# Optimization experiments

Measured on AMD Instinct MI355X. Metric: run time of the kernel, lower is better.

Reference implementation:

```python
import jax, jax.numpy as jnp
import numpy as np

B, T_TEXT, T_MEL = 8, 256, 1024
VOCAB, MEL, H = 256, 80, 512
NH, HD = 8, 64  # MultiheadAttention: 8 heads, head_dim 64


def _linear(x, w, b):
    return x @ w.T + b


def _lstm(x, w_ih, w_hh, b_ih, b_hh, reverse=False):
    # torch LSTM, gate order i,f,g,o; x: [B,T,Din] -> [B,T,H]
    xg = jnp.einsum('bti,gi->btg', x, w_ih) + b_ih  # precompute input contributions
    h0 = jnp.zeros((x.shape[0], w_hh.shape[1]), x.dtype)

    def step(carry, xt):
        h, c = carry
        g = xt + h @ w_hh.T + b_hh
        i, f, gg, o = jnp.split(g, 4, axis=-1)
        c = jax.nn.sigmoid(f) * c + jax.nn.sigmoid(i) * jnp.tanh(gg)
        h = jax.nn.sigmoid(o) * jnp.tanh(c)
        return (h, c), h

    _, hs = jax.lax.scan(step, (h0, h0), jnp.swapaxes(xg, 0, 1), reverse=reverse)
    return jnp.swapaxes(hs, 0, 1)


def _length_regulate(enc, durations, max_len):
    # Vectorized equivalent of the nested python loop: token j owns output
    # positions [cum[j-1], cum[j]); padded positions are zero, mask True=pad.
    dur = jnp.round(durations).astype(jnp.int32)
    cum = jnp.cumsum(dur, axis=1)                              # [B,T_text]
    pos = jnp.arange(max_len)                                  # [max_len]
    idx = jax.vmap(lambda c: jnp.searchsorted(c, pos, side='right'))(cum)
    pad_mask = pos[None, :] >= cum[:, -1:]                     # True = padded
    idx = jnp.minimum(idx, enc.shape[1] - 1)
    exp = jnp.take_along_axis(enc, idx[..., None], axis=1)     # [B,max_len,H]
    exp = exp * (~pad_mask)[..., None].astype(enc.dtype)
    return exp, pad_mask


def setup_inputs() -> dict:
    key = jax.random.key(0)
    ks = jax.random.split(key, 40)

    def rn(k, shape, scale=0.02):
        return jax.random.normal(k, shape, jnp.float32) * scale

    inp = {}
    inp['phoneme_indices'] = jax.random.randint(ks[0], (B, T_TEXT), 0, VOCAB)
    inp['mel_specs'] = jax.random.normal(ks[1], (B, T_MEL, MEL), jnp.float32)
    inp['phoneme_durations'] = jax.random.randint(ks[2], (B, T_TEXT), 0, 8).astype(jnp.float32)
    # parameters
    inp['emb'] = rn(ks[3], (VOCAB, H), 1.0)
    inp['enc_w_ih_f'] = rn(ks[4], (4 * H, H))
    inp['enc_w_hh_f'] = rn(ks[5], (4 * H, H))
    inp['enc_b_ih_f'] = rn(ks[6], (4 * H,))
    inp['enc_b_hh_f'] = rn(ks[7], (4 * H,))
    inp['enc_w_ih_b'] = rn(ks[8], (4 * H, H))
    inp['enc_w_hh_b'] = rn(ks[9], (4 * H, H))
    inp['enc_b_ih_b'] = rn(ks[10], (4 * H,))
    inp['enc_b_hh_b'] = rn(ks[11], (4 * H,))
    inp['proj_w'] = rn(ks[12], (H, 2 * H))
    inp['proj_b'] = rn(ks[13], (H,))
    inp['dur_w1'] = rn(ks[14], (H, H))
    inp['dur_b1'] = rn(ks[15], (H,))
    inp['dur_w2'] = rn(ks[16], (H // 2, H))
    inp['dur_b2'] = rn(ks[17], (H // 2,))
    inp['dur_w3'] = rn(ks[18], (1, H // 2))
    inp['dur_b3'] = rn(ks[19], (1,))
    inp['mel_in_w'] = rn(ks[20], (H, MEL))
    inp['mel_in_b'] = rn(ks[21], (H,))
    inp['attn_in_w'] = rn(ks[22], (3 * H, H))
    inp['attn_in_b'] = rn(ks[23], (3 * H,))
    inp['attn_out_w'] = rn(ks[24], (H, H))
    inp['attn_out_b'] = rn(ks[25], (H,))
    inp['dec_w_ih'] = rn(ks[26], (4 * H, 2 * H))
    inp['dec_w_hh'] = rn(ks[27], (4 * H, H))
    inp['dec_b_ih'] = rn(ks[28], (4 * H,))
    inp['dec_b_hh'] = rn(ks[29], (4 * H,))
    inp['mel_out_w'] = rn(ks[30], (MEL, H))
    inp['mel_out_b'] = rn(ks[31], (MEL,))
    return inp


def reference(phoneme_indices, mel_specs, phoneme_durations, emb,
              enc_w_ih_f, enc_w_hh_f, enc_b_ih_f, enc_b_hh_f,
              enc_w_ih_b, enc_w_hh_b, enc_b_ih_b, enc_b_hh_b,
              proj_w, proj_b, dur_w1, dur_b1, dur_w2, dur_b2, dur_w3, dur_b3,
              mel_in_w, mel_in_b, attn_in_w, attn_in_b, attn_out_w, attn_out_b,
              dec_w_ih, dec_w_hh, dec_b_ih, dec_b_hh, mel_out_w, mel_out_b):
    b = phoneme_indices.shape[0]
    # encode_text (dropout = identity in eval)
    x = emb[phoneme_indices]                                   # [B,T_text,H]
    hf = _lstm(x, enc_w_ih_f, enc_w_hh_f, enc_b_ih_f, enc_b_hh_f)
    hb = _lstm(x, enc_w_ih_b, enc_w_hh_b, enc_b_ih_b, enc_b_hh_b, reverse=True)
    enc = _linear(jnp.concatenate([hf, hb], axis=-1), proj_w, proj_b)
    # duration predictor
    h1 = jax.nn.relu(_linear(enc, dur_w1, dur_b1))
    h2 = jax.nn.relu(_linear(h1, dur_w2, dur_b2))
    log_dur = _linear(h2, dur_w3, dur_b3)[..., 0]              # [B,T_text]
    # length regulation to mel length
    exp, pad_mask = _length_regulate(enc, phoneme_durations, mel_specs.shape[1])
    # teacher-forced decoder: queries depend only on shifted mel targets,
    # so the per-timestep attention loop == one batched MHA over all steps.
    mel_in = jnp.concatenate([jnp.zeros_like(mel_specs[:, :1]), mel_specs[:, :-1]], axis=1)
    q_in = _linear(mel_in, mel_in_w, mel_in_b)                 # [B,T_mel,H]
    wq, wk, wv = jnp.split(attn_in_w, 3, axis=0)
    bq, bk, bv = jnp.split(attn_in_b, 3, axis=0)
    q = _linear(q_in, wq, bq).reshape(b, -1, NH, HD)
    k = _linear(exp, wk, bk).reshape(b, -1, NH, HD)
    v = _linear(exp, wv, bv).reshape(b, -1, NH, HD)
    scores = jnp.einsum('bqhd,bkhd->bhqk', q, k) / np.sqrt(HD).astype(np.float32)
    scores = jnp.where(pad_mask[:, None, None, :], jnp.asarray(-1e9, scores.dtype), scores)
    attn = jax.nn.softmax(scores, axis=-1)
    ctx = jnp.einsum('bhqk,bkhd->bqhd', attn, v).reshape(b, -1, H)
    attended = _linear(ctx, attn_out_w, attn_out_b)
    # decoder LSTM over full sequence (the only true recurrence)
    dec_in = jnp.concatenate([q_in, attended], axis=-1)        # [B,T_mel,2H]
    dec_out = _lstm(dec_in, dec_w_ih, dec_w_hh, dec_b_ih, dec_b_hh)
    mel_pred = _linear(dec_out, mel_out_w, mel_out_b)          # [B,T_mel,MEL]
    return mel_pred, log_dur
```

## Files before the change

kernel.cpp:

```cpp
#include <hip/hip_runtime.h>
#include <hip/hip_bf16.h>


typedef unsigned short u16;
typedef unsigned int u32;
typedef unsigned long long u64;
typedef short short8 __attribute__((ext_vector_type(8)));
typedef float float4_ __attribute__((ext_vector_type(4)));

__device__ __forceinline__ u16 f2b16(float f) {
  u32 u = __float_as_uint(f);
  u = (u + 0x7FFF + ((u >> 16) & 1)) >> 16;
  return (u16)u;
}
__device__ __forceinline__ float b2f(u16 h) { return __uint_as_float((u32)h << 16); }
__device__ __forceinline__ float sigm(float x) { return 1.f / (1.f + __expf(-x)); }
__device__ __forceinline__ float tanh_(float x) { return 2.f / (1.f + __expf(-2.f * x)) - 1.f; }

__global__ void f2b_k(const float* __restrict__ s, u16* __restrict__ d, int n) {
  for (int i = blockIdx.x * 256 + threadIdx.x; i < n; i += gridDim.x * 256) d[i] = f2b16(s[i]);
}
__global__ void permconv_k(const float* __restrict__ s, u16* __restrict__ d, int K) {
  int row = blockIdx.x; int u = row >> 2, G = row & 3;
  const float* sr = s + (long)(G * 512 + u) * K;
  u16* dr = d + (long)row * K;
  for (int c = threadIdx.x; c < K; c += 256) dr[c] = f2b16(sr[c]);
}
__global__ void biascomb_k(const float* __restrict__ bih, const float* __restrict__ bhh,
                           float* __restrict__ out) {
  int r = blockIdx.x * 256 + threadIdx.x;
  int u = r >> 2, G = r & 3;
  out[r] = bih[G * 512 + u] + bhh[G * 512 + u];
}
__global__ void melinw_k(const float* __restrict__ s, u16* __restrict__ d) {
  int row = blockIdx.x, c = threadIdx.x;
  d[row * 128 + c] = (c < 80) ? f2b16(s[row * 80 + c]) : (u16)0;
}
__global__ void meloutw_k(const float* __restrict__ s, u16* __restrict__ d) {
  int row = blockIdx.x;
  for (int c = threadIdx.x; c < 512; c += 256)
    d[row * 512 + c] = (row < 80) ? f2b16(s[row * 512 + c]) : (u16)0;
}
__global__ void biaspad_k(const float* __restrict__ s, float* __restrict__ d) {
  int t = threadIdx.x;
  d[t] = (t < 80) ? s[t] : 0.f;
}
__global__ void embed_k(const int* __restrict__ pid, const float* __restrict__ emb,
                        u16* __restrict__ x) {
  int t = blockIdx.x, b = blockIdx.y;
  int row = pid[b * 256 + t];
  const float* e = emb + (long)row * 512;
  u16* xr = x + ((long)b * 256 + t) * 512;
  xr[threadIdx.x] = f2b16(e[threadIdx.x]);
  xr[threadIdx.x + 256] = f2b16(e[threadIdx.x + 256]);
}
__global__ void melin_k(const float* __restrict__ mel, u16* __restrict__ out) {
  int t = blockIdx.x, b = blockIdx.y, c = threadIdx.x;
  float v = (c < 80 && t > 0) ? mel[((long)b * 1024 + (t - 1)) * 80 + c] : 0.f;
  out[((long)b * 1024 + t) * 128 + c] = f2b16(v);
}
__global__ void cumsum_k(const float* __restrict__ dur, int* __restrict__ cum,
                         int* __restrict__ Lb) {
  int b = blockIdx.x, t = threadIdx.x;
  __shared__ int sd[256];
  sd[t] = __float2int_rn(dur[b * 256 + t]);
  __syncthreads();
  for (int o = 1; o < 256; o <<= 1) {
    int v = (t >= o) ? sd[t - o] : 0;
    __syncthreads();
    sd[t] += v;
    __syncthreads();
  }
  cum[b * 256 + t] = sd[t];
  if (t == 255) Lb[b] = min(sd[255], 1024);
}
__global__ void gather_k(const int* __restrict__ cum, const u16* __restrict__ enc,
                         u16* __restrict__ exp_) {
  int pos = blockIdx.x, b = blockIdx.y;
  const int* cb = cum + b * 256;
  int last = cb[255];
  u32 val = 0;
  if (pos < last) {
    int lo = 0, hi = 255;
    while (lo < hi) { int mid = (lo + hi) >> 1; if (cb[mid] > pos) hi = mid; else lo = mid + 1; }
    val = ((const u32*)(enc + ((long)b * 256 + lo) * 512))[threadIdx.x];
  }
  ((u32*)(exp_ + ((long)b * 1024 + pos) * 512))[threadIdx.x] = val;
}
__global__ void softmax_k(const float* __restrict__ sbuf, u16* __restrict__ P,
                          const int* __restrict__ Lb) {
  int qp = blockIdx.x, b = blockIdx.y;
  const float* s = sbuf + ((long)b * 1024 + qp) * 1024;
  u16* p = P + ((long)b * 1024 + qp) * 1024;
  int L = Lb[b];
  __shared__ float red[256];
  int tid = threadIdx.x;
  float m = -1e30f;
  for (int i = tid; i < L; i += 256) m = fmaxf(m, s[i]);
  red[tid] = m; __syncthreads();
  for (int o = 128; o > 0; o >>= 1) { if (tid < o) red[tid] = fmaxf(red[tid], red[tid + o]); __syncthreads(); }
  float mx = red[0];
  __syncthreads();
  float sm = 0.f;
  for (int i = tid; i < L; i += 256) sm += __expf(s[i] - mx);
  red[tid] = sm; __syncthreads();
  for (int o = 128; o > 0; o >>= 1) { if (tid < o) red[tid] += red[tid + o]; __syncthreads(); }
  float inv = 1.f / red[0];
  for (int i = tid; i < 1024; i += 256) {
    float v = (i < L) ? __expf(s[i] - mx) * inv : 0.f;
    p[i] = f2b16(v);
  }
}
__global__ void dur3_k(const u16* __restrict__ h2, const float* __restrict__ w3,
                       const float* __restrict__ b3, float* __restrict__ out) {
  int row = blockIdx.x * 4 + (threadIdx.x >> 6);
  int l = threadIdx.x & 63;
  const u16* hr = h2 + (long)row * 256;
  float s = 0.f;
  for (int i = 0; i < 4; i++) { int c = l * 4 + i; s += b2f(hr[c]) * w3[c]; }
  for (int o = 32; o > 0; o >>= 1) s += __shfl_down(s, o);
  if (l == 0) out[row] = s + b3[0];
}

__global__ __launch_bounds__(256) void gemm_bt(
    const u16* __restrict__ A, const u16* __restrict__ A2, int ksplit, int lda, int lda2, long sA,
    const u16* __restrict__ B, int ldb, long sB, void* __restrict__ Cv, int ldc, long sC,
    const float* __restrict__ bias, float alpha, int N, int K, int flags) {
  __shared__ u16 As[128 * 72];
  __shared__ u16 Bs[128 * 72];
  int z = blockIdx.z;
  const u16* Ab = A + (long)z * sA;
  const u16* A2b = A2 ? (A2 + (long)z * sA) : (const u16*)0;
  const u16* Bb = B + (long)z * sB;
  int m0 = blockIdx.x * 128, n0 = blockIdx.y * 128;
  int tid = threadIdx.x, wave = tid >> 6, lane = tid & 63;
  int wm = wave & 1, wn = wave >> 1;
  int nl = lane & 15, kb = (lane >> 4) * 8, ml = (lane >> 4) * 4;
  float4_ acc[4][4];
  for (int i = 0; i < 4; i++)
    for (int j = 0; j < 4; j++) { acc[i][j][0] = 0; acc[i][j][1] = 0; acc[i][j][2] = 0; acc[i][j][3] = 0; }
  int rr = tid >> 3, cc = (tid & 7) * 8;
  for (int k0 = 0; k0 < K; k0 += 64) {
    int gk = k0 + cc;
#pragma unroll
    for (int i = 0; i < 4; i++) {
      int row = rr + i * 32;
      const u16* sa = (gk < ksplit) ? (Ab + (long)(m0 + row) * lda + gk)
                                    : (A2b + (long)(m0 + row) * lda2 + (gk - ksplit));
      *(short8*)&As[row * 72 + cc] = *(const short8*)sa;
      *(short8*)&Bs[row * 72 + cc] = *(const short8*)(Bb + (long)(n0 + row) * ldb + gk);
    }
    __syncthreads();
#pragma unroll
    for (int kk = 0; kk < 64; kk += 32) {
      short8 af[4], bfr[4];
#pragma unroll
      for (int i = 0; i < 4; i++) af[i] = *(const short8*)&As[(wm * 64 + i * 16 + nl) * 72 + kk + kb];
#pragma unroll
      for (int i = 0; i < 4; i++) bfr[i] = *(const short8*)&Bs[(wn * 64 + i * 16 + nl) * 72 + kk + kb];
#pragma unroll
      for (int mi = 0; mi < 4; mi++)
#pragma unroll
        for (int ni = 0; ni < 4; ni++)
          acc[mi][ni] = __builtin_amdgcn_mfma_f32_16x16x32_bf16(af[mi], bfr[ni], acc[mi][ni], 0, 0, 0);
    }
    __syncthreads();
  }
  for (int ni = 0; ni < 4; ni++) {
    int n = n0 + wn * 64 + ni * 16 + nl;
    if (n >= N) continue;
    float bv = bias ? bias[n] : 0.f;
    for (int mi = 0; mi < 4; mi++) {
#pragma unroll
      for (int r = 0; r < 4; r++) {
        int m = m0 + wm * 64 + mi * 16 + ml + r;
        float v = acc[mi][ni][r] * alpha + bv;
        if (flags & 2) v = fmaxf(v, 0.f);
        long idx = (flags & 4) ? ((long)n * ldc + m) : ((long)m * ldc + n);
        if (flags & 1) ((u16*)Cv)[z * sC + idx] = f2b16(v);
        else ((float*)Cv)[z * sC + idx] = v;
      }
    }
  }
}


__global__ __launch_bounds__(256) void enc_rec_k(
    const float* __restrict__ xg_f, const float* __restrict__ xg_b,
    const u16* __restrict__ whh_f, const u16* __restrict__ whh_b,
    u16* __restrict__ hcat, u64* __restrict__ hglob) {
  int dir = blockIdx.x >> 5, wg = blockIdx.x & 31;
  int tid = threadIdx.x, wave = tid >> 6, lane = tid & 63;
  int nl = lane & 15, kb = (lane >> 4) * 8, ml = (lane >> 4) * 4;
  int nt = wg * 4 + wave;
  const float* xg = dir ? xg_b : xg_f;
  const u16* whh = dir ? whh_b : whh_f;
  u64* hg = hglob + dir * 4096;
  __shared__ u16 h_s[2][16 * 520];
  __shared__ float gbuf[4][16][17];
  __shared__ float c_s[4][4][8];
  short8 warr[16];
  {
    const u16* wr = whh + (long)(wg * 64 + wave * 16 + nl) * 512 + kb;
#pragma unroll
    for (int kc = 0; kc < 16; kc++) warr[kc] = *(const short8*)(wr + kc * 32);
  }
  if (lane < 32) c_s[wave][lane & 3][lane >> 2] = 0.f;
  __syncthreads();
  float nxt[4];
  {
    int t0 = dir ? 255 : 0;
#pragma unroll
    for (int r = 0; r < 4; r++) {
      int m = ml + r;
      nxt[r] = (m < 8) ? xg[((long)m * 256 + t0) * 2048 + nt * 16 + nl] : 0.f;
    }
  }
  int prow = tid >> 5, c32 = tid & 31;
  for (int s = 0; s < 256; ++s) {
    int t = dir ? 255 - s : s;
    int pb = s & 1;
    float cur0 = nxt[0], cur1 = nxt[1], cur2 = nxt[2], cur3 = nxt[3];
    if (s > 0) {
      const u64* hp = hg + (long)pb * 2048 + prow * 256 + c32 * 2;
      u64 a[8];
      u32 tg = (u32)s;
      for (;;) {
#pragma unroll
        for (int j = 0; j < 4; j++) {
          a[2 * j] = __hip_atomic_load(hp + j * 64, __ATOMIC_RELAXED, __HIP_MEMORY_SCOPE_AGENT);
          a[2 * j + 1] =
              __hip_atomic_load(hp + j * 64 + 1, __ATOMIC_RELAXED, __HIP_MEMORY_SCOPE_AGENT);
        }
        u32 bad = 0;
#pragma unroll
        for (int i = 0; i < 8; i++) bad |= ((u32)(a[i] >> 32) ^ tg);
        if (!bad) break;
      }
      u64* dp = (u64*)(h_s[pb] + prow * 520);
#pragma unroll
      for (int j = 0; j < 4; j++)
        dp[c32 + j * 32] = (a[2 * j] & 0xffffffffull) | (a[2 * j + 1] << 32);
    }
    __syncthreads();
    if (s + 1 < 256) {
      int tn = dir ? 255 - (s + 1) : (s + 1);
#pragma unroll
      for (int r = 0; r < 4; r++) {
        int m = ml + r;
        nxt[r] = (m < 8) ? xg[((long)m * 256 + tn) * 2048 + nt * 16 + nl] : 0.f;
      }
    }
    float4_ ac0, ac1, ac2, ac3;
    ac0[0] = cur0; ac0[1] = cur1; ac0[2] = cur2; ac0[3] = cur3;
    ac1[0] = 0; ac1[1] = 0; ac1[2] = 0; ac1[3] = 0;
    ac2 = ac1; ac3 = ac1;
    if (s > 0) {
      const u16* hrow = h_s[pb] + nl * 520 + kb;
#pragma unroll
      for (int kc = 0; kc < 16; kc += 4) {
        ac0 = __builtin_amdgcn_mfma_f32_16x16x32_bf16(
            *(const short8*)(hrow + (kc + 0) * 32), warr[kc + 0], ac0, 0, 0, 0);
        ac1 = __builtin_amdgcn_mfma_f32_16x16x32_bf16(
            *(const short8*)(hrow + (kc + 1) * 32), warr[kc + 1], ac1, 0, 0, 0);
        ac2 = __builtin_amdgcn_mfma_f32_16x16x32_bf16(
            *(const short8*)(hrow + (kc + 2) * 32), warr[kc + 2], ac2, 0, 0, 0);
        ac3 = __builtin_amdgcn_mfma_f32_16x16x32_bf16(
            *(const short8*)(hrow + (kc + 3) * 32), warr[kc + 3], ac3, 0, 0, 0);
      }
    }
    float4_ acc = (ac0 + ac1) + (ac2 + ac3);
    gbuf[wave][nl][ml + 0] = acc[0];
    gbuf[wave][nl][ml + 1] = acc[1];
    gbuf[wave][nl][ml + 2] = acc[2];
    gbuf[wave][nl][ml + 3] = acc[3];
    if (lane < 32) {
      int ul = lane & 3, b = lane >> 2;
      float gi = gbuf[wave][ul * 4 + 0][b];
      float gf = gbuf[wave][ul * 4 + 1][b];
      float gg = gbuf[wave][ul * 4 + 2][b];
      float go = gbuf[wave][ul * 4 + 3][b];
      float c = c_s[wave][ul][b];
      c = sigm(gf) * c + sigm(gi) * tanh_(gg);
      float h = sigm(go) * tanh_(c);
      c_s[wave][ul][b] = c;
      int u = nt * 4 + ul;
      u16 hb2 = f2b16(h);
      u32 partner = (u32)__shfl_down((int)hb2, 1);
      if ((ul & 1) == 0) {
        u32 pair = (u32)hb2 | (partner << 16);
        *(u32*)&hcat[((long)b * 256 + t) * 1024 + dir * 512 + u] = pair;
        u64 word = (u64)pair | ((u64)(u32)(s + 1) << 32);
        __hip_atomic_store(hg + (long)((s + 1) & 1) * 2048 + b * 256 + (u >> 1), word,
                           __ATOMIC_RELAXED, __HIP_MEMORY_SCOPE_AGENT);
      }
    }
  }
}

__global__ __launch_bounds__(256) void dec_rec_k(
    const float* __restrict__ xg, const u16* __restrict__ whh,
    u16* __restrict__ dec_out, u64* __restrict__ hglob) {
  int wg = blockIdx.x;
  int tid = threadIdx.x, wave = tid >> 6, lane = tid & 63;
  int nl = lane & 15, kb = (lane >> 4) * 8, ml = (lane >> 4) * 4;
  int nt = wg * 4 + wave;
  __shared__ u16 h_s[2][16 * 520];
  __shared__ float gbuf[4][16][17];
  __shared__ float c_s[4][4][8];
  short8 warr[16];
  {
    const u16* wr = whh + (long)(wg * 64 + wave * 16 + nl) * 512 + kb;
#pragma unroll
    for (int kc = 0; kc < 16; kc++) warr[kc] = *(const short8*)(wr + kc * 32);
  }
  if (lane < 32) c_s[wave][lane & 3][lane >> 2] = 0.f;
  __syncthreads();
  float nxt[4];
#pragma unroll
  for (int r = 0; r < 4; r++) {
    int m = ml + r;
    nxt[r] = (m < 8) ? xg[((long)m * 1024 + 0) * 2048 + nt * 16 + nl] : 0.f;
  }
  int prow = tid >> 5, c32 = tid & 31;
  for (int s = 0; s < 1024; ++s) {
    int pb = s & 1;
    float cur0 = nxt[0], cur1 = nxt[1], cur2 = nxt[2], cur3 = nxt[3];
    if (s > 0) {
      const u64* hp = hglob + (long)pb * 2048 + prow * 256 + c32 * 2;
      u64 a[8];
      u32 tg = (u32)s;
      for (;;) {
#pragma unroll
        for (int j = 0; j < 4; j++) {
          a[2 * j] = __hip_atomic_load(hp + j * 64, __ATOMIC_RELAXED, __HIP_MEMORY_SCOPE_AGENT);
          a[2 * j + 1] =
              __hip_atomic_load(hp + j * 64 + 1, __ATOMIC_RELAXED, __HIP_MEMORY_SCOPE_AGENT);
        }
        u32 bad = 0;
#pragma unroll
        for (int i = 0; i < 8; i++) bad |= ((u32)(a[i] >> 32) ^ tg);
        if (!bad) break;
      }
      u64* dp = (u64*)(h_s[pb] + prow * 520);
#pragma unroll
      for (int j = 0; j < 4; j++)
        dp[c32 + j * 32] = (a[2 * j] & 0xffffffffull) | (a[2 * j + 1] << 32);
    }
    __syncthreads();
    if (s + 1 < 1024) {
#pragma unroll
      for (int r = 0; r < 4; r++) {
        int m = ml + r;
        nxt[r] = (m < 8) ? xg[((long)m * 1024 + (s + 1)) * 2048 + nt * 16 + nl] : 0.f;
      }
    }
    float4_ ac0, ac1, ac2, ac3;
    ac0[0] = cur0; ac0[1] = cur1; ac0[2] = cur2; ac0[3] = cur3;
    ac1[0] = 0; ac1[1] = 0; ac1[2] = 0; ac1[3] = 0;
    ac2 = ac1; ac3 = ac1;
    if (s > 0) {
      const u16* hrow = h_s[pb] + nl * 520 + kb;
#pragma unroll
      for (int kc = 0; kc < 16; kc += 4) {
        ac0 = __builtin_amdgcn_mfma_f32_16x16x32_bf16(
            *(const short8*)(hrow + (kc + 0) * 32), warr[kc + 0], ac0, 0, 0, 0);
        ac1 = __builtin_amdgcn_mfma_f32_16x16x32_bf16(
            *(const short8*)(hrow + (kc + 1) * 32), warr[kc + 1], ac1, 0, 0, 0);
        ac2 = __builtin_amdgcn_mfma_f32_16x16x32_bf16(
            *(const short8*)(hrow + (kc + 2) * 32), warr[kc + 2], ac2, 0, 0, 0);
        ac3 = __builtin_amdgcn_mfma_f32_16x16x32_bf16(
            *(const short8*)(hrow + (kc + 3) * 32), warr[kc + 3], ac3, 0, 0, 0);
      }
    }
    float4_ acc = (ac0 + ac1) + (ac2 + ac3);
    gbuf[wave][nl][ml + 0] = acc[0];
    gbuf[wave][nl][ml + 1] = acc[1];
    gbuf[wave][nl][ml + 2] = acc[2];
    gbuf[wave][nl][ml + 3] = acc[3];
    if (lane < 32) {
      int ul = lane & 3, b = lane >> 2;
      float gi = gbuf[wave][ul * 4 + 0][b];
      float gf = gbuf[wave][ul * 4 + 1][b];
      float gg = gbuf[wave][ul * 4 + 2][b];
      float go = gbuf[wave][ul * 4 + 3][b];
      float c = c_s[wave][ul][b];
      c = sigm(gf) * c + sigm(gi) * tanh_(gg);
      float h = sigm(go) * tanh_(c);
      c_s[wave][ul][b] = c;
      int u = nt * 4 + ul;
      u16 hb2 = f2b16(h);
      u32 partner = (u32)__shfl_down((int)hb2, 1);
      if ((ul & 1) == 0) {
        u32 pair = (u32)hb2 | (partner << 16);
        *(u32*)&dec_out[((long)b * 1024 + s) * 512 + u] = pair;
        u64 word = (u64)pair | ((u64)(u32)(s + 1) << 32);
        __hip_atomic_store(hglob + (long)((s + 1) & 1) * 2048 + b * 256 + (u >> 1), word,
                           __ATOMIC_RELAXED, __HIP_MEMORY_SCOPE_AGENT);
      }
    }
  }
}

extern "C" void kernel_launch(void* const* d_in, const int* in_sizes, int n_in,
                              void* d_out, int out_size, void* d_ws, size_t ws_size,
                              hipStream_t stream) {
  (void)in_sizes; (void)n_in; (void)out_size; (void)ws_size;
  const int* pid = (const int*)d_in[0];
  const float* mel = (const float*)d_in[1];
  const float* dur = (const float*)d_in[2];
  const float* emb = (const float*)d_in[3];
  const float* e_ihf = (const float*)d_in[4];
  const float* e_hhf = (const float*)d_in[5];
  const float* e_bihf = (const float*)d_in[6];
  const float* e_bhhf = (const float*)d_in[7];
  const float* e_ihb = (const float*)d_in[8];
  const float* e_hhb = (const float*)d_in[9];
  const float* e_bihb = (const float*)d_in[10];
  const float* e_bhhb = (const float*)d_in[11];
  const float* proj_w = (const float*)d_in[12];
  const float* proj_b = (const float*)d_in[13];
  const float* dw1 = (const float*)d_in[14];
  const float* db1 = (const float*)d_in[15];
  const float* dw2 = (const float*)d_in[16];
  const float* db2 = (const float*)d_in[17];
  const float* dw3 = (const float*)d_in[18];
  const float* db3 = (const float*)d_in[19];
  const float* miw = (const float*)d_in[20];
  const float* mib = (const float*)d_in[21];
  const float* aiw = (const float*)d_in[22];
  const float* aib = (const float*)d_in[23];
  const float* aow = (const float*)d_in[24];
  const float* aob = (const float*)d_in[25];
  const float* d_ih = (const float*)d_in[26];
  const float* d_hh = (const float*)d_in[27];
  const float* d_bih = (const float*)d_in[28];
  const float* d_bhh = (const float*)d_in[29];
  const float* mow = (const float*)d_in[30];
  const float* mob = (const float*)d_in[31];
  float* out = (float*)d_out;

  char* W = (char*)d_ws;
  constexpr size_t o_xgf = 0;
  constexpr size_t o_xgb = o_xgf + 16777216;
  constexpr size_t o_sbuf = o_xgb + 16777216;
  constexpr size_t o_decxg = o_xgf;
  constexpr size_t o_pool = o_sbuf + 33554432;
  constexpr size_t o_x = o_pool;
  constexpr size_t o_hcat = o_x + 2097152;
  constexpr size_t o_dh1 = o_hcat + 4194304;
  constexpr size_t o_dh2 = o_dh1 + 2097152;
  constexpr size_t o_melin = o_dh2 + 1048576;
  constexpr size_t o_att = o_pool;
  constexpr size_t o_enc = o_melin + 2097152;
  constexpr size_t o_exp = o_enc + 2097152;
  constexpr size_t o_ctx = o_exp;
  constexpr size_t o_qin = o_exp + 8388608;
  constexpr size_t o_q = o_qin + 8388608;
  constexpr size_t o_decout = o_q;
  constexpr size_t o_k = o_q + 8388608;
  constexpr size_t o_vt = o_k + 8388608;
  constexpr size_t o_p = o_vt + 8519680;
  constexpr size_t o_w0 = o_p + 16777216;
  constexpr size_t o_w_eihf = o_w0;
  constexpr size_t o_w_eihb = o_w_eihf + 2097152;
  constexpr size_t o_w_ehhf = o_w_eihb + 2097152;
  constexpr size_t o_w_ehhb = o_w_ehhf + 2097152;
  constexpr size_t o_w_dih = o_w_ehhb + 2097152;
  constexpr size_t o_w_dhh = o_w_dih + 4194304;
  constexpr size_t o_w_proj = o_w_dhh + 2097152;
  constexpr size_t o_w_d1 = o_w_proj + 1048576;
  constexpr size_t o_w_d2 = o_w_d1 + 524288;
  constexpr size_t o_w_ai = o_w_d2 + 262144;
  constexpr size_t o_w_ao = o_w_ai + 1572864;
  constexpr size_t o_w_mi = o_w_ao + 524288;
  constexpr size_t o_w_mo = o_w_mi + 131072;
  constexpr size_t o_bc_ef = o_w_mo + 131072;
  constexpr size_t o_bc_eb = o_bc_ef + 8192;
  constexpr size_t o_bc_d = o_bc_eb + 8192;
  constexpr size_t o_b_mo = o_bc_d + 8192;
  constexpr size_t o_cum = o_b_mo + 512;
  constexpr size_t o_lb = o_cum + 8192;
  constexpr size_t o_hge = o_lb + 256;
  constexpr size_t o_hgd = o_hge + 65536;

  hipMemsetAsync(W + o_hge, 0, 98304, stream);

  f2b_k<<<512, 256, 0, stream>>>(proj_w, (u16*)(W + o_w_proj), 512 * 1024);
  f2b_k<<<512, 256, 0, stream>>>(dw1, (u16*)(W + o_w_d1), 512 * 512);
  f2b_k<<<256, 256, 0, stream>>>(dw2, (u16*)(W + o_w_d2), 256 * 512);
  f2b_k<<<512, 256, 0, stream>>>(aiw, (u16*)(W + o_w_ai), 1536 * 512);
  f2b_k<<<512, 256, 0, stream>>>(aow, (u16*)(W + o_w_ao), 512 * 512);
  permconv_k<<<2048, 256, 0, stream>>>(e_ihf, (u16*)(W + o_w_eihf), 512);
  permconv_k<<<2048, 256, 0, stream>>>(e_ihb, (u16*)(W + o_w_eihb), 512);
  permconv_k<<<2048, 256, 0, stream>>>(e_hhf, (u16*)(W + o_w_ehhf), 512);
  permconv_k<<<2048, 256, 0, stream>>>(e_hhb, (u16*)(W + o_w_ehhb), 512);
  permconv_k<<<2048, 256, 0, stream>>>(d_ih, (u16*)(W + o_w_dih), 1024);
  permconv_k<<<2048, 256, 0, stream>>>(d_hh, (u16*)(W + o_w_dhh), 512);
  biascomb_k<<<8, 256, 0, stream>>>(e_bihf, e_bhhf, (float*)(W + o_bc_ef));
  biascomb_k<<<8, 256, 0, stream>>>(e_bihb, e_bhhb, (float*)(W + o_bc_eb));
  biascomb_k<<<8, 256, 0, stream>>>(d_bih, d_bhh, (float*)(W + o_bc_d));
  melinw_k<<<512, 128, 0, stream>>>(miw, (u16*)(W + o_w_mi));
  meloutw_k<<<128, 256, 0, stream>>>(mow, (u16*)(W + o_w_mo));
  biaspad_k<<<1, 128, 0, stream>>>(mob, (float*)(W + o_b_mo));

  auto gemm = [&](size_t oA, size_t oA2, int ksplit, int lda, int lda2, long sA, size_t oB,
                  int ldb, long sB, void* C, int ldc, long sC, const float* bias, float alpha,
                  int M, int N, int K, int flags, int batch) {
    dim3 g(M / 128, (N + 127) / 128, batch);
    gemm_bt<<<g, 256, 0, stream>>>((const u16*)(W + oA),
                                   oA2 ? (const u16*)(W + oA2) : (const u16*)0, ksplit, lda, lda2,
                                   sA, (const u16*)(W + oB), ldb, sB, C, ldc, sC, bias, alpha, N,
                                   K, flags);
  };

  embed_k<<<dim3(256, 8), 256, 0, stream>>>(pid, emb, (u16*)(W + o_x));
  gemm(o_x, 0, 512, 512, 0, 0, o_w_eihf, 512, 0, W + o_xgf, 2048, 0,
       (const float*)(W + o_bc_ef), 1.f, 2048, 2048, 512, 0, 1);
  gemm(o_x, 0, 512, 512, 0, 0, o_w_eihb, 512, 0, W + o_xgb, 2048, 0,
       (const float*)(W + o_bc_eb), 1.f, 2048, 2048, 512, 0, 1);
  enc_rec_k<<<64, 256, 0, stream>>>((const float*)(W + o_xgf), (const float*)(W + o_xgb),
                                    (const u16*)(W + o_w_ehhf), (const u16*)(W + o_w_ehhb),
                                    (u16*)(W + o_hcat), (u64*)(W + o_hge));
  gemm(o_hcat, 0, 1024, 1024, 0, 0, o_w_proj, 1024, 0, W + o_enc, 512, 0, proj_b, 1.f, 2048, 512,
       1024, 1, 1);
  gemm(o_enc, 0, 512, 512, 0, 0, o_w_d1, 512, 0, W + o_dh1, 512, 0, db1, 1.f, 2048, 512, 512, 3, 1);
  gemm(o_dh1, 0, 512, 512, 0, 0, o_w_d2, 512, 0, W + o_dh2, 256, 0, db2, 1.f, 2048, 256, 512, 3, 1);
  dur3_k<<<512, 256, 0, stream>>>((const u16*)(W + o_dh2), dw3, db3, out + 655360);
  cumsum_k<<<8, 256, 0, stream>>>(dur, (int*)(W + o_cum), (int*)(W + o_lb));
  gather_k<<<dim3(1024, 8), 256, 0, stream>>>((const int*)(W + o_cum), (const u16*)(W + o_enc),
                                              (u16*)(W + o_exp));
  melin_k<<<dim3(1024, 8), 128, 0, stream>>>(mel, (u16*)(W + o_melin));
  gemm(o_melin, 0, 128, 128, 0, 0, o_w_mi, 128, 0, W + o_qin, 512, 0, mib, 1.f, 8192, 512, 128, 1, 1);
  gemm(o_qin, 0, 512, 512, 0, 0, o_w_ai, 512, 0, W + o_q, 512, 0, aib, 1.f, 8192, 512, 512, 1, 1);
  gemm(o_exp, 0, 512, 512, 0, 0, o_w_ai + (size_t)512 * 512 * 2, 512, 0, W + o_k, 512, 0,
       aib + 512, 1.f, 8192, 512, 512, 1, 1);
  gemm(o_exp, 0, 512, 512, 0, 524288, o_w_ai + (size_t)1024 * 512 * 2, 512, 0, W + o_vt, 1024,
       524288, aib + 1024, 1.f, 1024, 512, 512, 5, 8);
  for (int h = 0; h < 8; h++) {
    gemm(o_q + (size_t)h * 128, 0, 64, 512, 0, 524288, o_k + (size_t)h * 128, 512, 524288,
         W + o_sbuf, 1024, 1048576, (const float*)0, 0.125f, 1024, 1024, 64, 0, 8);
    softmax_k<<<dim3(1024, 8), 256, 0, stream>>>((const float*)(W + o_sbuf), (u16*)(W + o_p),
                                                 (const int*)(W + o_lb));
    gemm(o_p, 0, 1024, 1024, 0, 1048576, o_vt + (size_t)h * 64 * 1024 * 2, 1024, 524288,
         (u16*)(W + o_ctx) + h * 64, 512, 524288, (const float*)0, 1.f, 1024, 64, 1024, 1, 8);
  }
  gemm(o_ctx, 0, 512, 512, 0, 0, o_w_ao, 512, 0, W + o_att, 512, 0, aob, 1.f, 8192, 512, 512, 1, 1);
  gemm(o_qin, o_att, 512, 512, 512, 0, o_w_dih, 1024, 0, W + o_decxg, 2048, 0,
       (const float*)(W + o_bc_d), 1.f, 8192, 2048, 1024, 0, 1);
  dec_rec_k<<<32, 256, 0, stream>>>((const float*)(W + o_decxg), (const u16*)(W + o_w_dhh),
                                    (u16*)(W + o_decout), (u64*)(W + o_hgd));
  gemm(o_decout, 0, 512, 512, 0, 0, o_w_mo, 512, 0, d_out, 80, 0, (const float*)(W + o_b_mo), 1.f,
       8192, 80, 512, 0, 1);
}
```

Before: 3.141 ms.

## Halve recurrent LSTM workgroups by giving each wave two gate tiles

Each wave in the encoder and decoder recurrence kernels now owns two 16-column tiles of W_hh, 8 hidden units instead of 4, held in registers. The grids shrink from 64 to 32 blocks for the encoder and from 32 to 16 for the decoder. This cuts how many workgroups take part in the per-timestep global-memory spin barrier, and shares each h-tile LDS read across two MFMAs. In exchange it doubles register pressure for weights and the per-wave MFMA and gate work on the serial critical path.

New measurement: 3.508 ms. 11.7% more time.

```diff
diff --git a/kernel.cpp b/kernel.cpp
--- a/kernel.cpp
+++ b/kernel.cpp
@@ -189,38 +189,44 @@
     const float* __restrict__ xg_f, const float* __restrict__ xg_b,
     const u16* __restrict__ whh_f, const u16* __restrict__ whh_b,
     u16* __restrict__ hcat, u64* __restrict__ hglob) {
-  int dir = blockIdx.x >> 5, wg = blockIdx.x & 31;
+  int dir = blockIdx.x >> 4, wg = blockIdx.x & 15;
   int tid = threadIdx.x, wave = tid >> 6, lane = tid & 63;
   int nl = lane & 15, kb = (lane >> 4) * 8, ml = (lane >> 4) * 4;
-  int nt = wg * 4 + wave;
+  int gw = wg * 4 + wave;
   const float* xg = dir ? xg_b : xg_f;
   const u16* whh = dir ? whh_b : whh_f;
   u64* hg = hglob + dir * 4096;
   __shared__ u16 h_s[2][16 * 520];
-  __shared__ float gbuf[4][16][17];
-  __shared__ float c_s[4][4][8];
-  short8 warr[16];
+  __shared__ float gbuf[4][2][16][17];
+  __shared__ float c_s[4][8][8];
+  short8 w0[16], w1[16];
   {
-    const u16* wr = whh + (long)(wg * 64 + wave * 16 + nl) * 512 + kb;
-#pragma unroll
-    for (int kc = 0; kc < 16; kc++) warr[kc] = *(const short8*)(wr + kc * 32);
-  }
-  if (lane < 32) c_s[wave][lane & 3][lane >> 2] = 0.f;
+    const u16* wr0 = whh + (long)((2 * gw + 0) * 16 + nl) * 512 + kb;
+    const u16* wr1 = whh + (long)((2 * gw + 1) * 16 + nl) * 512 + kb;
+#pragma unroll
+    for (int kc = 0; kc < 16; kc++) {
+      w0[kc] = *(const short8*)(wr0 + kc * 32);
+      w1[kc] = *(const short8*)(wr1 + kc * 32);
+    }
+  }
+  c_s[wave][lane & 7][lane >> 3] = 0.f;
   __syncthreads();
-  float nxt[4];
+  float nxt0[4], nxt1[4];
   {
     int t0 = dir ? 255 : 0;
 #pragma unroll
     for (int r = 0; r < 4; r++) {
       int m = ml + r;
-      nxt[r] = (m < 8) ? xg[((long)m * 256 + t0) * 2048 + nt * 16 + nl] : 0.f;
+      nxt0[r] = (m < 8) ? xg[((long)m * 256 + t0) * 2048 + (2 * gw + 0) * 16 + nl] : 0.f;
+      nxt1[r] = (m < 8) ? xg[((long)m * 256 + t0) * 2048 + (2 * gw + 1) * 16 + nl] : 0.f;
     }
   }
   int prow = tid >> 5, c32 = tid & 31;
   for (int s = 0; s < 256; ++s) {
     int t = dir ? 255 - s : s;
     int pb = s & 1;
-    float cur0 = nxt[0], cur1 = nxt[1], cur2 = nxt[2], cur3 = nxt[3];
+    float cu00 = nxt0[0], cu01 = nxt0[1], cu02 = nxt0[2], cu03 = nxt0[3];
+    float cu10 = nxt1[0], cu11 = nxt1[1], cu12 = nxt1[2], cu13 = nxt1[3];
     if (s > 0) {
       const u64* hp = hg + (long)pb * 2048 + prow * 256 + c32 * 2;
       u64 a[8];
@@ -248,43 +254,45 @@
 #pragma unroll
       for (int r = 0; r < 4; r++) {
         int m = ml + r;
-        nxt[r] = (m < 8) ? xg[((long)m * 256 + tn) * 2048 + nt * 16 + nl] : 0.f;
-      }
-    }
-    float4_ ac0, ac1, ac2, ac3;
-    ac0[0] = cur0; ac0[1] = cur1; ac0[2] = cur2; ac0[3] = cur3;
-    ac1[0] = 0; ac1[1] = 0; ac1[2] = 0; ac1[3] = 0;
-    ac2 = ac1; ac3 = ac1;
+        nxt0[r] = (m < 8) ? xg[((long)m * 256 + tn) * 2048 + (2 * gw + 0) * 16 + nl] : 0.f;
+        nxt1[r] = (m < 8) ? xg[((long)m * 256 + tn) * 2048 + (2 * gw + 1) * 16 + nl] : 0.f;
+      }
+    }
+    float4_ a00, a01, a10, a11;
+    a00[0] = cu00; a00[1] = cu01; a00[2] = cu02; a00[3] = cu03;
+    a10[0] = cu10; a10[1] = cu11; a10[2] = cu12; a10[3] = cu13;
+    a01[0] = 0; a01[1] = 0; a01[2] = 0; a01[3] = 0;
+    a11 = a01;
     if (s > 0) {
       const u16* hrow = h_s[pb] + nl * 520 + kb;
 #pragma unroll
-      for (int kc = 0; kc < 16; kc += 4) {
-        ac0 = __builtin_amdgcn_mfma_f32_16x16x32_bf16(
-            *(const short8*)(hrow + (kc + 0) * 32), warr[kc + 0], ac0, 0, 0, 0);
-        ac1 = __builtin_amdgcn_mfma_f32_16x16x32_bf16(
-            *(const short8*)(hrow + (kc + 1) * 32), warr[kc + 1], ac1, 0, 0, 0);
-        ac2 = __builtin_amdgcn_mfma_f32_16x16x32_bf16(
-            *(const short8*)(hrow + (kc + 2) * 32), warr[kc + 2], ac2, 0, 0, 0);
-        ac3 = __builtin_amdgcn_mfma_f32_16x16x32_bf16(
-            *(const short8*)(hrow + (kc + 3) * 32), warr[kc + 3], ac3, 0, 0, 0);
-      }
-    }
-    float4_ acc = (ac0 + ac1) + (ac2 + ac3);
-    gbuf[wave][nl][ml + 0] = acc[0];
-    gbuf[wave][nl][ml + 1] = acc[1];
-    gbuf[wave][nl][ml + 2] = acc[2];
-    gbuf[wave][nl][ml + 3] = acc[3];
-    if (lane < 32) {
-      int ul = lane & 3, b = lane >> 2;
-      float gi = gbuf[wave][ul * 4 + 0][b];
-      float gf = gbuf[wave][ul * 4 + 1][b];
-      float gg = gbuf[wave][ul * 4 + 2][b];
-      float go = gbuf[wave][ul * 4 + 3][b];
+      for (int kc = 0; kc < 16; kc += 2) {
+        short8 hA = *(const short8*)(hrow + (kc + 0) * 32);
+        short8 hB = *(const short8*)(hrow + (kc + 1) * 32);
+        a00 = __builtin_amdgcn_mfma_f32_16x16x32_bf16(hA, w0[kc + 0], a00, 0, 0, 0);
+        a10 = __builtin_amdgcn_mfma_f32_16x16x32_bf16(hA, w1[kc + 0], a10, 0, 0, 0);
+        a01 = __builtin_amdgcn_mfma_f32_16x16x32_bf16(hB, w0[kc + 1], a01, 0, 0, 0);
+        a11 = __builtin_amdgcn_mfma_f32_16x16x32_bf16(hB, w1[kc + 1], a11, 0, 0, 0);
+      }
+    }
+    float4_ acc0 = a00 + a01;
+    float4_ acc1 = a10 + a11;
+#pragma unroll
+    for (int r = 0; r < 4; r++) {
+      gbuf[wave][0][nl][ml + r] = acc0[r];
+      gbuf[wave][1][nl][ml + r] = acc1[r];
+    }
+    {
+      int ul = lane & 7, b = lane >> 3, ti = ul >> 2, q = ul & 3;
+      float gi = gbuf[wave][ti][q * 4 + 0][b];
+      float gf = gbuf[wave][ti][q * 4 + 1][b];
+      float gg = gbuf[wave][ti][q * 4 + 2][b];
+      float go = gbuf[wave][ti][q * 4 + 3][b];
       float c = c_s[wave][ul][b];
       c = sigm(gf) * c + sigm(gi) * tanh_(gg);
       float h = sigm(go) * tanh_(c);
       c_s[wave][ul][b] = c;
-      int u = nt * 4 + ul;
+      int u = gw * 8 + ul;
       u16 hb2 = f2b16(h);
       u32 partner = (u32)__shfl_down((int)hb2, 1);
       if ((ul & 1) == 0) {
@@ -304,28 +312,34 @@
   int wg = blockIdx.x;
   int tid = threadIdx.x, wave = tid >> 6, lane = tid & 63;
   int nl = lane & 15, kb = (lane >> 4) * 8, ml = (lane >> 4) * 4;
-  int nt = wg * 4 + wave;
+  int gw = wg * 4 + wave;
   __shared__ u16 h_s[2][16 * 520];
-  __shared__ float gbuf[4][16][17];
-  __shared__ float c_s[4][4][8];
-  short8 warr[16];
+  __shared__ float gbuf[4][2][16][17];
+  __shared__ float c_s[4][8][8];
+  short8 w0[16], w1[16];
   {
-    const u16* wr = whh + (long)(wg * 64 + wave * 16 + nl) * 512 + kb;
-#pragma unroll
-    for (int kc = 0; kc < 16; kc++) warr[kc] = *(const short8*)(wr + kc * 32);
-  }
-  if (lane < 32) c_s[wave][lane & 3][lane >> 2] = 0.f;
+    const u16* wr0 = whh + (long)((2 * gw + 0) * 16 + nl) * 512 + kb;
+    const u16* wr1 = whh + (long)((2 * gw + 1) * 16 + nl) * 512 + kb;
+#pragma unroll
+    for (int kc = 0; kc < 16; kc++) {
+      w0[kc] = *(const short8*)(wr0 + kc * 32);
+      w1[kc] = *(const short8*)(wr1 + kc * 32);
+    }
+  }
+  c_s[wave][lane & 7][lane >> 3] = 0.f;
   __syncthreads();
-  float nxt[4];
+  float nxt0[4], nxt1[4];
 #pragma unroll
   for (int r = 0; r < 4; r++) {
     int m = ml + r;
-    nxt[r] = (m < 8) ? xg[((long)m * 1024 + 0) * 2048 + nt * 16 + nl] : 0.f;
+    nxt0[r] = (m < 8) ? xg[((long)m * 1024 + 0) * 2048 + (2 * gw + 0) * 16 + nl] : 0.f;
+    nxt1[r] = (m < 8) ? xg[((long)m * 1024 + 0) * 2048 + (2 * gw + 1) * 16 + nl] : 0.f;
   }
   int prow = tid >> 5, c32 = tid & 31;
   for (int s = 0; s < 1024; ++s) {
     int pb = s & 1;
-    float cur0 = nxt[0], cur1 = nxt[1], cur2 = nxt[2], cur3 = nxt[3];
+    float cu00 = nxt0[0], cu01 = nxt0[1], cu02 = nxt0[2], cu03 = nxt0[3];
+    float cu10 = nxt1[0], cu11 = nxt1[1], cu12 = nxt1[2], cu13 = nxt1[3];
     if (s > 0) {
       const u64* hp = hglob + (long)pb * 2048 + prow * 256 + c32 * 2;
       u64 a[8];
@@ -352,43 +366,45 @@
 #pragma unroll
       for (int r = 0; r < 4; r++) {
         int m = ml + r;
-        nxt[r] = (m < 8) ? xg[((long)m * 1024 + (s + 1)) * 2048 + nt * 16 + nl] : 0.f;
-      }
-    }
-    float4_ ac0, ac1, ac2, ac3;
-    ac0[0] = cur0; ac0[1] = cur1; ac0[2] = cur2; ac0[3] = cur3;
-    ac1[0] = 0; ac1[1] = 0; ac1[2] = 0; ac1[3] = 0;
-    ac2 = ac1; ac3 = ac1;
+        nxt0[r] = (m < 8) ? xg[((long)m * 1024 + (s + 1)) * 2048 + (2 * gw + 0) * 16 + nl] : 0.f;
+        nxt1[r] = (m < 8) ? xg[((long)m * 1024 + (s + 1)) * 2048 + (2 * gw + 1) * 16 + nl] : 0.f;
+      }
+    }
+    float4_ a00, a01, a10, a11;
+    a00[0] = cu00; a00[1] = cu01; a00[2] = cu02; a00[3] = cu03;
+    a10[0] = cu10; a10[1] = cu11; a10[2] = cu12; a10[3] = cu13;
+    a01[0] = 0; a01[1] = 0; a01[2] = 0; a01[3] = 0;
+    a11 = a01;
     if (s > 0) {
       const u16* hrow = h_s[pb] + nl * 520 + kb;
 #pragma unroll
-      for (int kc = 0; kc < 16; kc += 4) {
-        ac0 = __builtin_amdgcn_mfma_f32_16x16x32_bf16(
-            *(const short8*)(hrow + (kc + 0) * 32), warr[kc + 0], ac0, 0, 0, 0);
-        ac1 = __builtin_amdgcn_mfma_f32_16x16x32_bf16(
-            *(const short8*)(hrow + (kc + 1) * 32), warr[kc + 1], ac1, 0, 0, 0);
-        ac2 = __builtin_amdgcn_mfma_f32_16x16x32_bf16(
-            *(const short8*)(hrow + (kc + 2) * 32), warr[kc + 2], ac2, 0, 0, 0);
-        ac3 = __builtin_amdgcn_mfma_f32_16x16x32_bf16(
-            *(const short8*)(hrow + (kc + 3) * 32), warr[kc + 3], ac3, 0, 0, 0);
-      }
-    }
-    float4_ acc = (ac0 + ac1) + (ac2 + ac3);
-    gbuf[wave][nl][ml + 0] = acc[0];
-    gbuf[wave][nl][ml + 1] = acc[1];
-    gbuf[wave][nl][ml + 2] = acc[2];
-    gbuf[wave][nl][ml + 3] = acc[3];
-    if (lane < 32) {
-      int ul = lane & 3, b = lane >> 2;
-      float gi = gbuf[wave][ul * 4 + 0][b];
-      float gf = gbuf[wave][ul * 4 + 1][b];
-      float gg = gbuf[wave][ul * 4 + 2][b];
-      float go = gbuf[wave][ul * 4 + 3][b];
+      for (int kc = 0; kc < 16; kc += 2) {
+        short8 hA = *(const short8*)(hrow + (kc + 0) * 32);
+        short8 hB = *(const short8*)(hrow + (kc + 1) * 32);
+        a00 = __builtin_amdgcn_mfma_f32_16x16x32_bf16(hA, w0[kc + 0], a00, 0, 0, 0);
+        a10 = __builtin_amdgcn_mfma_f32_16x16x32_bf16(hA, w1[kc + 0], a10, 0, 0, 0);
+        a01 = __builtin_amdgcn_mfma_f32_16x16x32_bf16(hB, w0[kc + 1], a01, 0, 0, 0);
+        a11 = __builtin_amdgcn_mfma_f32_16x16x32_bf16(hB, w1[kc + 1], a11, 0, 0, 0);
+      }
+    }
+    float4_ acc0 = a00 + a01;
+    float4_ acc1 = a10 + a11;
+#pragma unroll
+    for (int r = 0; r < 4; r++) {
+      gbuf[wave][0][nl][ml + r] = acc0[r];
+      gbuf[wave][1][nl][ml + r] = acc1[r];
+    }
+    {
+      int ul = lane & 7, b = lane >> 3, ti = ul >> 2, q = ul & 3;
+      float gi = gbuf[wave][ti][q * 4 + 0][b];
+      float gf = gbuf[wave][ti][q * 4 + 1][b];
+      float gg = gbuf[wave][ti][q * 4 + 2][b];
+      float go = gbuf[wave][ti][q * 4 + 3][b];
       float c = c_s[wave][ul][b];
       c = sigm(gf) * c + sigm(gi) * tanh_(gg);
       float h = sigm(go) * tanh_(c);
       c_s[wave][ul][b] = c;
-      int u = nt * 4 + ul;
+      int u = gw * 8 + ul;
       u16 hb2 = f2b16(h);
       u32 partner = (u32)__shfl_down((int)hb2, 1);
       if ((ul & 1) == 0) {
@@ -519,7 +535,7 @@
        (const float*)(W + o_bc_ef), 1.f, 2048, 2048, 512, 0, 1);
   gemm(o_x, 0, 512, 512, 0, 0, o_w_eihb, 512, 0, W + o_xgb, 2048, 0,
        (const float*)(W + o_bc_eb), 1.f, 2048, 2048, 512, 0, 1);
-  enc_rec_k<<<64, 256, 0, stream>>>((const float*)(W + o_xgf), (const float*)(W + o_xgb),
+  enc_rec_k<<<32, 256, 0, stream>>>((const float*)(W + o_xgf), (const float*)(W + o_xgb),
                                     (const u16*)(W + o_w_ehhf), (const u16*)(W + o_w_ehhb),
                                     (u16*)(W + o_hcat), (u64*)(W + o_hge));
   gemm(o_hcat, 0, 1024, 1024, 0, 0, o_w_proj, 1024, 0, W + o_enc, 512, 0, proj_b, 1.f, 2048, 512,
@@ -548,7 +564,7 @@
   gemm(o_ctx, 0, 512, 512, 0, 0, o_w_ao, 512, 0, W + o_att, 512, 0, aob, 1.f, 8192, 512, 512, 1, 1);
   gemm(o_qin, o_att, 512, 512, 512, 0, o_w_dih, 1024, 0, W + o_decxg, 2048, 0,
        (const float*)(W + o_bc_d), 1.f, 8192, 2048, 1024, 0, 1);
-  dec_rec_k<<<32, 256, 0, stream>>>((const float*)(W + o_decxg), (const u16*)(W + o_w_dhh),
+  dec_rec_k<<<16, 256, 0, stream>>>((const float*)(W + o_decxg), (const u16*)(W + o_w_dhh),
                                     (u16*)(W + o_decout), (u64*)(W + o_hgd));
   gemm(o_decout, 0, 512, 512, 0, 0, o_w_mo, 512, 0, d_out, 80, 0, (const float*)(W + o_b_mo), 1.f,
        8192, 80, 512, 0, 1);
```
